# Optimization experiments

Measured on AMD Instinct MI355X. Metric: run time of the kernel, lower is better.

## Reference

```python
import jax, jax.numpy as jnp
import numpy as np

_EPS = 1e-6
B, N, W, R, NW = 64, 1024, 64, 4, 1


def _cosine_weights(memory, keys, strengths):
    # memory: [B,N,W], keys: [B,H,W], strengths: [B,H] -> [B,H,N]
    dot = jnp.einsum('bhw,bnw->bhn', keys, memory)
    mem_norm = jnp.sqrt(jnp.sum(memory * memory, axis=-1) + _EPS)  # [B,N]
    key_norm = jnp.sqrt(jnp.sum(keys * keys, axis=-1) + _EPS)      # [B,H]
    sim = dot / (key_norm[:, :, None] * mem_norm[:, None, :] + _EPS)
    sharp = sim * jax.nn.softplus(strengths)[:, :, None]
    return jax.nn.softmax(sharp, axis=-1)


def _allocation(usage):
    # usage: [B,N] -> allocation weights [B,N] (DNC sort-based free-list)
    usage = _EPS + (1.0 - _EPS) * usage
    nonusage = 1.0 - usage
    sorted_nonusage, indices = jax.lax.top_k(nonusage, N)
    sorted_usage = 1.0 - sorted_nonusage
    prod_excl = jnp.concatenate(
        [jnp.ones_like(sorted_usage[:, :1]), jnp.cumprod(sorted_usage[:, :-1], axis=-1)], axis=-1)
    sorted_alloc = sorted_nonusage * prod_excl
    inv_perm = jnp.argsort(indices, axis=-1)  # batch_invert_permutation
    return jnp.take_along_axis(sorted_alloc, inv_perm, axis=-1)  # batch_gather


def _forward(memory, prev_read_weights, prev_write_weights, prev_usage, prev_link,
             prev_precedence, read_keys, read_strengths, write_keys, write_strengths,
             write_vectors, erase_vectors, free_gate, alloc_gate, write_gate, read_mode):
    # ---- usage update (Freeness.call); prev write weights are stop-gradient'd ----
    ww = jax.lax.stop_gradient(prev_write_weights)
    agg_write = 1.0 - jnp.prod(1.0 - ww, axis=1)                       # [B,N]
    usage = prev_usage + (1.0 - prev_usage) * agg_write
    phi = jnp.prod(1.0 - free_gate[:, :, None] * prev_read_weights, axis=1)
    usage = usage * phi
    # ---- write weights: content + allocation ----
    write_content = _cosine_weights(memory, write_keys, write_strengths)  # [B,NW,N]
    wg = alloc_gate * write_gate                                          # [B,NW]
    allocs = []
    u = usage
    for i in range(NW):  # fixed small head loop
        a = _allocation(u)
        allocs.append(a)
        u = u + (1.0 - u) * wg[:, i:i + 1] * a
    alloc_w = jnp.stack(allocs, axis=1)                                   # [B,NW,N]
    ag = alloc_gate[:, :, None]
    write_weights = write_gate[:, :, None] * (ag * alloc_w + (1.0 - ag) * write_content)
    # ---- erase + write memory ----
    reset = jnp.prod(1.0 - write_weights[:, :, :, None] * erase_vectors[:, :, None, :], axis=1)
    memory_new = memory * reset + jnp.einsum('bwn,bwk->bnk', write_weights, write_vectors)
    # ---- temporal link matrix update ----
    wi = write_weights[:, :, :, None]   # [B,NW,N,1]
    wj = write_weights[:, :, None, :]   # [B,NW,1,N]
    new_link = (1.0 - wi - wj) * prev_link + wi * prev_precedence[:, :, None, :]
    link = new_link * (1.0 - jnp.eye(N, dtype=memory.dtype))[None, None]  # zero diagonal
    # (precedence update, part of new state; not needed for read_words output)
    precedence = (1.0 - jnp.sum(write_weights, axis=-1, keepdims=True)) * prev_precedence + write_weights
    del precedence
    # ---- read weights: content + directional (forward/backward along link) ----
    read_content = _cosine_weights(memory_new, read_keys, read_strengths)   # [B,R,N]
    fwd_w = jnp.einsum('brm,bwnm->brwn', prev_read_weights, link)           # adjoint_b=True
    bwd_w = jnp.einsum('brm,bwmn->brwn', prev_read_weights, link)
    mode = jax.nn.softmax(read_mode, axis=-1)                                # [B,R,2*NW+1]
    backward_mode = mode[:, :, :NW]
    forward_mode = mode[:, :, NW:2 * NW]
    content_mode = mode[:, :, 2 * NW]
    read_weights = (content_mode[:, :, None] * read_content
                    + jnp.einsum('brw,brwn->brn', forward_mode, fwd_w)
                    + jnp.einsum('brw,brwn->brn', backward_mode, bwd_w))
    read_words = jnp.einsum('brn,bnw->brw', read_weights, memory_new)        # [B,R,W]
    return read_words


def setup_inputs() -> dict:
    key = jax.random.key(0)
    ks = jax.random.split(key, 16)
    rn = lambda k, s: jax.random.normal(k, s, jnp.float32)
    ru = lambda k, s: jax.random.uniform(k, s, dtype=jnp.float32)
    return {
        'memory': rn(ks[0], (B, N, W)),
        'prev_read_weights': ru(ks[1], (B, R, N)),
        'prev_write_weights': ru(ks[2], (B, NW, N)),
        'prev_usage': ru(ks[3], (B, N)),
        'prev_link': ru(ks[4], (B, NW, N, N)),
        'prev_precedence': ru(ks[5], (B, NW, N)),
        'read_keys': rn(ks[6], (B, R, W)),
        'read_strengths': rn(ks[7], (B, R)),
        'write_keys': rn(ks[8], (B, NW, W)),
        'write_strengths': rn(ks[9], (B, NW)),
        'write_vectors': rn(ks[10], (B, NW, W)),
        'erase_vectors': ru(ks[11], (B, NW, W)),
        'free_gate': ru(ks[12], (B, R)),
        'alloc_gate': ru(ks[13], (B, NW)),
        'write_gate': ru(ks[14], (B, NW)),
        'read_mode': rn(ks[15], (B, R, 2 * NW + 1)),
    }


def reference(memory, prev_read_weights, prev_write_weights, prev_usage, prev_link,
              prev_precedence, read_keys, read_strengths, write_keys, write_strengths,
              write_vectors, erase_vectors, free_gate, alloc_gate, write_gate, read_mode):
    return _forward(memory, prev_read_weights, prev_write_weights, prev_usage, prev_link,
                    prev_precedence, read_keys, read_strengths, write_keys, write_strengths,
                    write_vectors, erase_vectors, free_gate, alloc_gate, write_gate, read_mode)
```

## Files before the change

kernel.cpp:

```cpp
#include <hip/hip_runtime.h>
#include <cmath>

#define NN 1024
#define BB 64
#define WD 64
#define RR 4

constexpr float EPSF = 1e-6f;

__device__ __forceinline__ float softplusf(float x) {
    return fmaxf(x, 0.f) + log1pf(expf(-fabsf(x)));
}

__device__ __forceinline__ float block_sum(float v, float* red, float* bc) {
#pragma unroll
    for (int o = 1; o < 64; o <<= 1) v += __shfl_xor(v, o, 64);
    const int wid = threadIdx.x >> 6, lane = threadIdx.x & 63;
    if (lane == 0) red[wid] = v;
    __syncthreads();
    if (wid == 0) {
        float x = (lane < 16) ? red[lane] : 0.f;
#pragma unroll
        for (int o = 1; o < 16; o <<= 1) x += __shfl_xor(x, o, 64);
        if (lane == 0) bc[0] = x;
    }
    __syncthreads();
    return bc[0];
}

__device__ __forceinline__ float block_max(float v, float* red, float* bc) {
#pragma unroll
    for (int o = 1; o < 64; o <<= 1) v = fmaxf(v, __shfl_xor(v, o, 64));
    const int wid = threadIdx.x >> 6, lane = threadIdx.x & 63;
    if (lane == 0) red[wid] = v;
    __syncthreads();
    if (wid == 0) {
        float x = (lane < 16) ? red[lane] : -INFINITY;
#pragma unroll
        for (int o = 1; o < 16; o <<= 1) x = fmaxf(x, __shfl_xor(x, o, 64));
        if (lane == 0) bc[0] = x;
    }
    __syncthreads();
    return bc[0];
}

__device__ __forceinline__ float4 block_sum4(float4 v, float4* red, float4* bc) {
#pragma unroll
    for (int o = 1; o < 64; o <<= 1) {
        v.x += __shfl_xor(v.x, o, 64); v.y += __shfl_xor(v.y, o, 64);
        v.z += __shfl_xor(v.z, o, 64); v.w += __shfl_xor(v.w, o, 64);
    }
    const int wid = threadIdx.x >> 6, lane = threadIdx.x & 63;
    if (lane == 0) red[wid] = v;
    __syncthreads();
    if (wid == 0) {
        float4 x;
        if (lane < 16) x = red[lane];
        else { x.x = 0.f; x.y = 0.f; x.z = 0.f; x.w = 0.f; }
#pragma unroll
        for (int o = 1; o < 16; o <<= 1) {
            x.x += __shfl_xor(x.x, o, 64); x.y += __shfl_xor(x.y, o, 64);
            x.z += __shfl_xor(x.z, o, 64); x.w += __shfl_xor(x.w, o, 64);
        }
        if (lane == 0) bc[0] = x;
    }
    __syncthreads();
    return bc[0];
}

__device__ __forceinline__ float4 block_max4(float4 v, float4* red, float4* bc) {
#pragma unroll
    for (int o = 1; o < 64; o <<= 1) {
        v.x = fmaxf(v.x, __shfl_xor(v.x, o, 64)); v.y = fmaxf(v.y, __shfl_xor(v.y, o, 64));
        v.z = fmaxf(v.z, __shfl_xor(v.z, o, 64)); v.w = fmaxf(v.w, __shfl_xor(v.w, o, 64));
    }
    const int wid = threadIdx.x >> 6, lane = threadIdx.x & 63;
    if (lane == 0) red[wid] = v;
    __syncthreads();
    if (wid == 0) {
        float4 x;
        if (lane < 16) x = red[lane];
        else { x.x = -INFINITY; x.y = -INFINITY; x.z = -INFINITY; x.w = -INFINITY; }
#pragma unroll
        for (int o = 1; o < 16; o <<= 1) {
            x.x = fmaxf(x.x, __shfl_xor(x.x, o, 64)); x.y = fmaxf(x.y, __shfl_xor(x.y, o, 64));
            x.z = fmaxf(x.z, __shfl_xor(x.z, o, 64)); x.w = fmaxf(x.w, __shfl_xor(x.w, o, 64));
        }
        if (lane == 0) bc[0] = x;
    }
    __syncthreads();
    return bc[0];
}

__global__ __launch_bounds__(1024) void prep_kernel(
    const float* __restrict__ memory, const float* __restrict__ prw,
    const float* __restrict__ pww, const float* __restrict__ pusage,
    const float* __restrict__ pprec,
    const float* __restrict__ rkeys_g, const float* __restrict__ rstr_g,
    const float* __restrict__ wkeys_g, const float* __restrict__ wstr_g,
    const float* __restrict__ wvec_g, const float* __restrict__ evec_g,
    const float* __restrict__ fg_g, const float* __restrict__ ag_g,
    const float* __restrict__ wg_g,
    float* __restrict__ wwG, float* __restrict__ rcG,
    float* __restrict__ SrpG, float* __restrict__ SuwwG)
{
    __shared__ float wkey[WD], wvecS[WD], evecS[WD], rkey[RR * WD];
    __shared__ float skey[NN];
    __shared__ int   sidx[NN];
    __shared__ float pArr[NN], wcArr[NN], allocArr[NN];
    __shared__ float red1[16], bc1[1];
    __shared__ float4 red4[16], bc4[1];

    const int b = blockIdx.x, tid = threadIdx.x, n = tid;

    if (tid < WD) {
        wkey[tid]  = wkeys_g[b * WD + tid];
        wvecS[tid] = wvec_g[b * WD + tid];
        evecS[tid] = evec_g[b * WD + tid];
    } else if (tid >= 128 && tid < 128 + RR * WD) {
        int k = tid - 128;
        rkey[k] = rkeys_g[b * RR * WD + k];
    }
    __syncthreads();

    float ur[RR];
#pragma unroll
    for (int r = 0; r < RR; ++r) ur[r] = prw[((size_t)b * RR + r) * NN + n];
    const float pw = pww[b * NN + n];
    const float pu = pusage[b * NN + n];
    float usage = pu + (1.f - pu) * pw;
    float phi = 1.f;
#pragma unroll
    for (int r = 0; r < RR; ++r) phi *= (1.f - fg_g[b * RR + r] * ur[r]);
    usage *= phi;

    const float* mrow = memory + ((size_t)b * NN + n) * WD;
    float dot = 0.f, nrm = 0.f, knrm = 0.f;
#pragma unroll 4
    for (int w4 = 0; w4 < WD / 4; ++w4) {
        const float4 m = *(const float4*)(mrow + w4 * 4);
        const float4 k = *(const float4*)(wkey + w4 * 4);
        dot  += m.x * k.x + m.y * k.y + m.z * k.z + m.w * k.w;
        nrm  += m.x * m.x + m.y * m.y + m.z * m.z + m.w * m.w;
        knrm += k.x * k.x + k.y * k.y + k.z * k.z + k.w * k.w;
    }
    const float sim = dot / (sqrtf(knrm + EPSF) * sqrtf(nrm + EPSF) + EPSF);
    const float sharp = sim * softplusf(wstr_g[b]);
    const float mxw = block_max(sharp, red1, bc1);
    const float exw = expf(sharp - mxw);
    const float smw = block_sum(exw, red1, bc1);
    wcArr[n] = exw / smw;

    const float ue = EPSF + (1.f - EPSF) * usage;
    skey[n] = 1.f - ue;
    sidx[n] = n;
    __syncthreads();
    for (int k = 2; k <= NN; k <<= 1) {
        for (int j = k >> 1; j > 0; j >>= 1) {
            const int ixj = tid ^ j;
            if (ixj > tid) {
                const float ka = skey[tid], kb = skey[ixj];
                const int ia = sidx[tid], ib = sidx[ixj];
                const bool precBA = (kb > ka) || (kb == ka && ib < ia);
                const bool precAB = (ka > kb) || (ka == kb && ia < ib);
                const bool dosw = ((tid & k) == 0) ? precBA : precAB;
                if (dosw) { skey[tid] = kb; skey[ixj] = ka; sidx[tid] = ib; sidx[ixj] = ia; }
            }
            __syncthreads();
        }
    }
    pArr[n] = (n == 0) ? 1.f : (1.f - skey[n - 1]);
    __syncthreads();
    for (int off = 1; off < NN; off <<= 1) {
        const float t = (n >= off) ? pArr[n - off] : 1.f;
        __syncthreads();
        pArr[n] *= t;
        __syncthreads();
    }
    allocArr[sidx[n]] = skey[n] * pArr[n];
    __syncthreads();

    const float agv = ag_g[b], wgv = wg_g[b];
    const float ww = wgv * (agv * allocArr[n] + (1.f - agv) * wcArr[n]);
    wwG[b * NN + n] = ww;

    float rdot0 = 0, rdot1 = 0, rdot2 = 0, rdot3 = 0, nn2 = 0;
    float rk0 = 0, rk1 = 0, rk2 = 0, rk3 = 0;
#pragma unroll 4
    for (int w4 = 0; w4 < WD / 4; ++w4) {
        const float4 m = *(const float4*)(mrow + w4 * 4);
        const float4 e = *(const float4*)(evecS + w4 * 4);
        const float4 v = *(const float4*)(wvecS + w4 * 4);
        float4 mn_;
        mn_.x = m.x * (1.f - ww * e.x) + ww * v.x;
        mn_.y = m.y * (1.f - ww * e.y) + ww * v.y;
        mn_.z = m.z * (1.f - ww * e.z) + ww * v.z;
        mn_.w = m.w * (1.f - ww * e.w) + ww * v.w;
        nn2 += mn_.x * mn_.x + mn_.y * mn_.y + mn_.z * mn_.z + mn_.w * mn_.w;
        const float4 k0 = *(const float4*)(rkey + 0 * WD + w4 * 4);
        const float4 k1 = *(const float4*)(rkey + 1 * WD + w4 * 4);
        const float4 k2 = *(const float4*)(rkey + 2 * WD + w4 * 4);
        const float4 k3 = *(const float4*)(rkey + 3 * WD + w4 * 4);
        rdot0 += k0.x * mn_.x + k0.y * mn_.y + k0.z * mn_.z + k0.w * mn_.w;
        rdot1 += k1.x * mn_.x + k1.y * mn_.y + k1.z * mn_.z + k1.w * mn_.w;
        rdot2 += k2.x * mn_.x + k2.y * mn_.y + k2.z * mn_.z + k2.w * mn_.w;
        rdot3 += k3.x * mn_.x + k3.y * mn_.y + k3.z * mn_.z + k3.w * mn_.w;
        rk0 += k0.x * k0.x + k0.y * k0.y + k0.z * k0.z + k0.w * k0.w;
        rk1 += k1.x * k1.x + k1.y * k1.y + k1.z * k1.z + k1.w * k1.w;
        rk2 += k2.x * k2.x + k2.y * k2.y + k2.z * k2.z + k2.w * k2.w;
        rk3 += k3.x * k3.x + k3.y * k3.y + k3.z * k3.z + k3.w * k3.w;
    }
    const float mnn = sqrtf(nn2 + EPSF);
    float4 sharp4;
    sharp4.x = rdot0 / (sqrtf(rk0 + EPSF) * mnn + EPSF) * softplusf(rstr_g[b * RR + 0]);
    sharp4.y = rdot1 / (sqrtf(rk1 + EPSF) * mnn + EPSF) * softplusf(rstr_g[b * RR + 1]);
    sharp4.z = rdot2 / (sqrtf(rk2 + EPSF) * mnn + EPSF) * softplusf(rstr_g[b * RR + 2]);
    sharp4.w = rdot3 / (sqrtf(rk3 + EPSF) * mnn + EPSF) * softplusf(rstr_g[b * RR + 3]);
    const float4 mx4 = block_max4(sharp4, red4, bc4);
    float4 e4;
    e4.x = expf(sharp4.x - mx4.x); e4.y = expf(sharp4.y - mx4.y);
    e4.z = expf(sharp4.z - mx4.z); e4.w = expf(sharp4.w - mx4.w);
    const float4 s4 = block_sum4(e4, red4, bc4);
    rcG[((size_t)b * RR + 0) * NN + n] = e4.x / s4.x;
    rcG[((size_t)b * RR + 1) * NN + n] = e4.y / s4.y;
    rcG[((size_t)b * RR + 2) * NN + n] = e4.z / s4.z;
    rcG[((size_t)b * RR + 3) * NN + n] = e4.w / s4.w;

    const float prec_n = pprec[b * NN + n];
    float4 sp4, sw4;
    sp4.x = ur[0] * prec_n; sp4.y = ur[1] * prec_n; sp4.z = ur[2] * prec_n; sp4.w = ur[3] * prec_n;
    const float4 SrpV = block_sum4(sp4, red4, bc4);
    sw4.x = ur[0] * ww; sw4.y = ur[1] * ww; sw4.z = ur[2] * ww; sw4.w = ur[3] * ww;
    const float4 SuwwV = block_sum4(sw4, red4, bc4);
    if (tid == 0) {
        SrpG[b * RR + 0] = SrpV.x; SrpG[b * RR + 1] = SrpV.y;
        SrpG[b * RR + 2] = SrpV.z; SrpG[b * RR + 3] = SrpV.w;
        SuwwG[b * RR + 0] = SuwwV.x; SuwwG[b * RR + 1] = SuwwV.y;
        SuwwG[b * RR + 2] = SuwwV.z; SuwwG[b * RR + 3] = SuwwV.w;
    }
}

__global__ __launch_bounds__(256) void link_kernel(
    const float* __restrict__ L, const float* __restrict__ prw,
    const float* __restrict__ wwG,
    float* __restrict__ rowU, float* __restrict__ rowV,
    float* __restrict__ colU, float* __restrict__ colV)
{
    __shared__ float uL[RR * NN];
    __shared__ float uwL[RR * NN];
    __shared__ float tile[64 * 68];

    const int b = blockIdx.y;
    const int n0 = blockIdx.x * 64;
    const int t = threadIdx.x;
    const int lane = t & 63;
    const int wid = t >> 6;

    for (int k = t; k < RR * NN; k += 256) {
        const float u = prw[(size_t)b * RR * NN + k];
        uL[k] = u;
        uwL[k] = u * wwG[b * NN + (k & (NN - 1))];
    }
    __syncthreads();

    const float* Lb = L + (size_t)b * NN * NN;
    float fuA = 0.f, fvA = 0.f;

    for (int tIdx = 0; tIdx < 16; ++tIdx) {
        const int m0 = tIdx * 64;
#pragma unroll
        for (int k = 0; k < 4; ++k) {
            const int f4 = t + k * 256;
            const int row = f4 >> 4, c4 = f4 & 15;
            const float4 v = *(const float4*)&Lb[(size_t)(n0 + row) * NN + m0 + c4 * 4];
            *(float4*)&tile[row * 68 + c4 * 4] = v;
        }
        __syncthreads();

#pragma unroll 4
        for (int g = 0; g < 16; ++g) {
            const float4 v  = *(const float4*)&tile[lane * 68 + g * 4];
            const float4 u  = *(const float4*)&uL[wid * NN + m0 + g * 4];
            const float4 uw = *(const float4*)&uwL[wid * NN + m0 + g * 4];
            fuA += v.x * u.x + v.y * u.y + v.z * u.z + v.w * u.w;
            fvA += v.x * uw.x + v.y * uw.y + v.z * uw.z + v.w * uw.w;
        }

        float cu = 0.f, cv = 0.f;
#pragma unroll 4
        for (int n4 = 0; n4 < 16; ++n4) {
            const float4 u  = *(const float4*)&uL[wid * NN + n0 + n4 * 4];
            const float4 uw = *(const float4*)&uwL[wid * NN + n0 + n4 * 4];
            const float v0 = tile[(n4 * 4 + 0) * 68 + lane];
            const float v1 = tile[(n4 * 4 + 1) * 68 + lane];
            const float v2 = tile[(n4 * 4 + 2) * 68 + lane];
            const float v3 = tile[(n4 * 4 + 3) * 68 + lane];
            cu += v0 * u.x + v1 * u.y + v2 * u.z + v3 * u.w;
            cv += v0 * uw.x + v1 * uw.y + v2 * uw.z + v3 * uw.w;
        }
        unsafeAtomicAdd(&colU[((size_t)b * RR + wid) * NN + m0 + lane], cu);
        unsafeAtomicAdd(&colV[((size_t)b * RR + wid) * NN + m0 + lane], cv);
        __syncthreads();
    }
    rowU[((size_t)b * RR + wid) * NN + n0 + lane] = fuA;
    rowV[((size_t)b * RR + wid) * NN + n0 + lane] = fvA;
}

__global__ __launch_bounds__(256) void combine_kernel(
    const float* __restrict__ memory, const float* __restrict__ prw,
    const float* __restrict__ pprec, const float* __restrict__ L,
    const float* __restrict__ evec_g, const float* __restrict__ wvec_g,
    const float* __restrict__ rmode_g,
    const float* __restrict__ wwG, const float* __restrict__ rcG,
    const float* __restrict__ rowU, const float* __restrict__ rowV,
    const float* __restrict__ colU, const float* __restrict__ colV,
    const float* __restrict__ SrpG, const float* __restrict__ SuwwG,
    float* __restrict__ out)
{
    __shared__ float rwL[RR][256];
    __shared__ float wwS[256];

    const int b = blockIdx.y;
    const int n0 = blockIdx.x * 256;
    const int t = threadIdx.x;
    const int n = n0 + t;

    const float wwn = wwG[b * NN + n];
    wwS[t] = wwn;
    const float prec_n = pprec[b * NN + n];
    const float diag = L[(size_t)b * NN * NN + (size_t)n * (NN + 1)];

#pragma unroll
    for (int r = 0; r < RR; ++r) {
        const size_t idx = ((size_t)b * RR + r) * NN + n;
        const float un = prw[idx];
        const float rc = rcG[idx];
        const float ru = rowU[idx], rv = rowV[idx];
        const float cuv = colU[idx], cvv = colV[idx];
        const float Srp = SrpG[b * RR + r], Suww = SuwwG[b * RR + r];
        const float corr = un * (1.f - 2.f * wwn) * diag;
        const float fwd = (1.f - wwn) * ru - rv - corr + wwn * (Srp - un * prec_n);
        const float bwd = (1.f - wwn) * cuv - cvv - corr + prec_n * (Suww - un * wwn);
        const float m0 = rmode_g[((size_t)b * RR + r) * 3 + 0];
        const float m1 = rmode_g[((size_t)b * RR + r) * 3 + 1];
        const float m2 = rmode_g[((size_t)b * RR + r) * 3 + 2];
        const float mx = fmaxf(m0, fmaxf(m1, m2));
        const float e0 = expf(m0 - mx), e1 = expf(m1 - mx), e2 = expf(m2 - mx);
        const float inv = 1.f / (e0 + e1 + e2);
        rwL[r][t] = (e2 * inv) * rc + (e1 * inv) * fwd + (e0 * inv) * bwd;
    }
    __syncthreads();

    const int r = t >> 6, w = t & 63;
    const float ev = evec_g[b * WD + w], wv = wvec_g[b * WD + w];
    float acc = 0.f;
    const float* mb = memory + ((size_t)b * NN + n0) * WD;
#pragma unroll 8
    for (int i = 0; i < 256; ++i) {
        const float m = mb[(size_t)i * WD + w];
        const float wwi = wwS[i];
        const float mn_ = m * (1.f - wwi * ev) + wwi * wv;
        acc += rwL[r][i] * mn_;
    }
    unsafeAtomicAdd(&out[((size_t)b * RR + r) * WD + w], acc);
}

extern "C" void kernel_launch(void* const* d_in, const int* in_sizes, int n_in,
                              void* d_out, int out_size, void* d_ws, size_t ws_size,
                              hipStream_t stream) {
    const float* memory = (const float*)d_in[0];
    const float* prw    = (const float*)d_in[1];
    const float* pww    = (const float*)d_in[2];
    const float* pusage = (const float*)d_in[3];
    const float* plink  = (const float*)d_in[4];
    const float* pprec  = (const float*)d_in[5];
    const float* rkeys  = (const float*)d_in[6];
    const float* rstr   = (const float*)d_in[7];
    const float* wkeys  = (const float*)d_in[8];
    const float* wstr   = (const float*)d_in[9];
    const float* wvec   = (const float*)d_in[10];
    const float* evec   = (const float*)d_in[11];
    const float* fg     = (const float*)d_in[12];
    const float* ag     = (const float*)d_in[13];
    const float* wg     = (const float*)d_in[14];
    const float* rmode  = (const float*)d_in[15];

    float* ws = (float*)d_ws;
    const size_t BN  = (size_t)BB * NN;
    const size_t BRN = (size_t)BB * RR * NN;
    float* wwG  = ws;
    float* rcG  = wwG + BN;
    float* rowU = rcG + BRN;
    float* rowV = rowU + BRN;
    float* colU = rowV + BRN;
    float* colV = colU + BRN;
    float* Srp  = colV + BRN;
    float* Suww = Srp + (size_t)BB * RR;

    hipMemsetAsync(colU, 0, 2 * BRN * sizeof(float), stream);
    hipMemsetAsync(d_out, 0, (size_t)out_size * sizeof(float), stream);

    prep_kernel<<<BB, 1024, 0, stream>>>(memory, prw, pww, pusage, pprec,
                                         rkeys, rstr, wkeys, wstr, wvec, evec,
                                         fg, ag, wg, wwG, rcG, Srp, Suww);
    link_kernel<<<dim3(16, BB), 256, 0, stream>>>(plink, prw, wwG,
                                                  rowU, rowV, colU, colV);
    combine_kernel<<<dim3(4, BB), 256, 0, stream>>>(memory, prw, pprec, plink,
                                                    evec, wvec, rmode,
                                                    wwG, rcG, rowU, rowV, colU, colV,
                                                    Srp, Suww, (float*)d_out);
}
```

Baseline: 596.1 us.

## Restructure link kernel into register-accumulated stripes with per-stripe column partials

```diff
diff --git a/kernel.cpp b/kernel.cpp
--- a/kernel.cpp
+++ b/kernel.cpp
@@ -5,11 +5,16 @@
 #define BB 64
 #define WD 64
 #define RR 4
+#define STRIPES 16
 
 constexpr float EPSF = 1e-6f;
 
 __device__ __forceinline__ float softplusf(float x) {
     return fmaxf(x, 0.f) + log1pf(expf(-fabsf(x)));
+}
+
+__device__ __forceinline__ float rfl(float x) {
+    return __int_as_float(__builtin_amdgcn_readfirstlane(__float_as_int(x)));
 }
 
 __device__ __forceinline__ float block_sum(float v, float* red, float* bc) {
@@ -101,7 +106,8 @@
     const float* __restrict__ wvec_g, const float* __restrict__ evec_g,
     const float* __restrict__ fg_g, const float* __restrict__ ag_g,
     const float* __restrict__ wg_g,
-    float* __restrict__ wwG, float* __restrict__ rcG,
+    float* __restrict__ wwG, float* __restrict__ uwGout,
+    float* __restrict__ rcG,
     float* __restrict__ SrpG, float* __restrict__ SuwwG)
 {
     __shared__ float wkey[WD], wvecS[WD], evecS[WD], rkey[RR * WD];
@@ -183,6 +189,9 @@
     const float agv = ag_g[b], wgv = wg_g[b];
     const float ww = wgv * (agv * allocArr[n] + (1.f - agv) * wcArr[n]);
     wwG[b * NN + n] = ww;
+#pragma unroll
+    for (int r = 0; r < RR; ++r)
+        uwGout[((size_t)b * RR + r) * NN + n] = ur[r] * ww;
 
     float rdot0 = 0, rdot1 = 0, rdot2 = 0, rdot3 = 0, nn2 = 0;
     float rk0 = 0, rk1 = 0, rk2 = 0, rk3 = 0;
@@ -240,70 +249,103 @@
     }
 }
 
-__global__ __launch_bounds__(256) void link_kernel(
+__global__ __launch_bounds__(1024) void link_kernel(
     const float* __restrict__ L, const float* __restrict__ prw,
-    const float* __restrict__ wwG,
-    float* __restrict__ rowU, float* __restrict__ rowV,
-    float* __restrict__ colU, float* __restrict__ colV)
+    const float* __restrict__ uwG,
+    float* __restrict__ rowP, float* __restrict__ colPart)
 {
-    __shared__ float uL[RR * NN];
-    __shared__ float uwL[RR * NN];
-    __shared__ float tile[64 * 68];
-
-    const int b = blockIdx.y;
-    const int n0 = blockIdx.x * 64;
-    const int t = threadIdx.x;
-    const int lane = t & 63;
-    const int wid = t >> 6;
-
-    for (int k = t; k < RR * NN; k += 256) {
-        const float u = prw[(size_t)b * RR * NN + k];
-        uL[k] = u;
-        uwL[k] = u * wwG[b * NN + (k & (NN - 1))];
-    }
-    __syncthreads();
-
-    const float* Lb = L + (size_t)b * NN * NN;
-    float fuA = 0.f, fvA = 0.f;
-
-    for (int tIdx = 0; tIdx < 16; ++tIdx) {
-        const int m0 = tIdx * 64;
-#pragma unroll
-        for (int k = 0; k < 4; ++k) {
-            const int f4 = t + k * 256;
-            const int row = f4 >> 4, c4 = f4 & 15;
-            const float4 v = *(const float4*)&Lb[(size_t)(n0 + row) * NN + m0 + c4 * 4];
-            *(float4*)&tile[row * 68 + c4 * 4] = v;
-        }
+    __shared__ float smem[16384];
+
+    const int s = blockIdx.x, b = blockIdx.y;
+    const int t = threadIdx.x, lane = t & 63, wid = t >> 6;
+
+#pragma unroll
+    for (int k = 0; k < 8; ++k) smem[t + k * 1024] = 0.f;
+    __syncthreads();
+
+    const int n0 = s * 64;
+    const int nb = n0 + wid * 4;
+
+    const float* vp[8];
+#pragma unroll
+    for (int r = 0; r < RR; ++r) {
+        vp[r]      = prw + (((size_t)b * RR + r) << 10);
+        vp[4 + r]  = uwG + (((size_t)b * RR + r) << 10);
+    }
+
+    float us[4][8];
+#pragma unroll
+    for (int rr = 0; rr < 4; ++rr)
+#pragma unroll
+        for (int v = 0; v < 8; ++v)
+            us[rr][v] = rfl(vp[v][nb + rr]);
+
+    float racc[4][8];
+#pragma unroll
+    for (int rr = 0; rr < 4; ++rr)
+#pragma unroll
+        for (int v = 0; v < 8; ++v) racc[rr][v] = 0.f;
+
+    const float* Lb = L + ((size_t)b << 20);
+
+    for (int cc = 0; cc < 16; ++cc) {
+        const int c = (cc + wid) & 15;
+        const int col = (c << 6) + lane;
+
+        float ul[8];
+#pragma unroll
+        for (int v = 0; v < 8; ++v) ul[v] = vp[v][col];
+
+        float cacc[8] = {0.f, 0.f, 0.f, 0.f, 0.f, 0.f, 0.f, 0.f};
+#pragma unroll
+        for (int rr = 0; rr < 4; ++rr) {
+            const float val = Lb[((size_t)(nb + rr) << 10) + col];
+#pragma unroll
+            for (int v = 0; v < 8; ++v) racc[rr][v] = fmaf(val, ul[v], racc[rr][v]);
+#pragma unroll
+            for (int v = 0; v < 8; ++v) cacc[v] = fmaf(val, us[rr][v], cacc[v]);
+        }
+#pragma unroll
+        for (int v = 0; v < 8; ++v)
+            unsafeAtomicAdd(&smem[(v << 10) + col], cacc[v]);
+    }
+    __syncthreads();
+
+    {
+        const size_t base = (((size_t)s * BB + b) * 8) << 10;
+#pragma unroll
+        for (int v = 0; v < 8; ++v)
+            colPart[base + (v << 10) + t] = smem[(v << 10) + t];
+    }
+    __syncthreads();
+
+#pragma unroll
+    for (int rd = 0; rd < 2; ++rd) {
+#pragma unroll
+        for (int row2 = 0; row2 < 2; ++row2)
+#pragma unroll
+            for (int v = 0; v < 8; ++v) {
+                const int q = row2 * 8 + v;
+                smem[(wid << 10) + (q << 6) + (lane ^ q)] = racc[rd * 2 + row2][v];
+            }
         __syncthreads();
-
-#pragma unroll 4
-        for (int g = 0; g < 16; ++g) {
-            const float4 v  = *(const float4*)&tile[lane * 68 + g * 4];
-            const float4 u  = *(const float4*)&uL[wid * NN + m0 + g * 4];
-            const float4 uw = *(const float4*)&uwL[wid * NN + m0 + g * 4];
-            fuA += v.x * u.x + v.y * u.y + v.z * u.z + v.w * u.w;
-            fvA += v.x * uw.x + v.y * uw.y + v.z * uw.z + v.w * uw.w;
-        }
-
-        float cu = 0.f, cv = 0.f;
-#pragma unroll 4
-        for (int n4 = 0; n4 < 16; ++n4) {
-            const float4 u  = *(const float4*)&uL[wid * NN + n0 + n4 * 4];
-            const float4 uw = *(const float4*)&uwL[wid * NN + n0 + n4 * 4];
-            const float v0 = tile[(n4 * 4 + 0) * 68 + lane];
-            const float v1 = tile[(n4 * 4 + 1) * 68 + lane];
-            const float v2 = tile[(n4 * 4 + 2) * 68 + lane];
-            const float v3 = tile[(n4 * 4 + 3) * 68 + lane];
-            cu += v0 * u.x + v1 * u.y + v2 * u.z + v3 * u.w;
-            cv += v0 * uw.x + v1 * uw.y + v2 * uw.z + v3 * uw.w;
-        }
-        unsafeAtomicAdd(&colU[((size_t)b * RR + wid) * NN + m0 + lane], cu);
-        unsafeAtomicAdd(&colV[((size_t)b * RR + wid) * NN + m0 + lane], cv);
+        const int q = lane >> 2;
+        const int sub = lane & 3;
+        float sum = 0.f;
+#pragma unroll
+        for (int i = 0; i < 16; ++i) {
+            const int j = sub * 16 + i;
+            sum += smem[(wid << 10) + (q << 6) + (j ^ q)];
+        }
+        sum += __shfl_xor(sum, 1, 64);
+        sum += __shfl_xor(sum, 2, 64);
+        if (sub == 0) {
+            const int v = q & 7, row2 = q >> 3;
+            const int n = n0 + wid * 4 + rd * 2 + row2;
+            rowP[(((size_t)b * 8 + v) << 10) + n] = sum;
+        }
         __syncthreads();
     }
-    rowU[((size_t)b * RR + wid) * NN + n0 + lane] = fuA;
-    rowV[((size_t)b * RR + wid) * NN + n0 + lane] = fvA;
 }
 
 __global__ __launch_bounds__(256) void combine_kernel(
@@ -312,8 +354,7 @@
     const float* __restrict__ evec_g, const float* __restrict__ wvec_g,
     const float* __restrict__ rmode_g,
     const float* __restrict__ wwG, const float* __restrict__ rcG,
-    const float* __restrict__ rowU, const float* __restrict__ rowV,
-    const float* __restrict__ colU, const float* __restrict__ colV,
+    const float* __restrict__ rowP, const float* __restrict__ colPart,
     const float* __restrict__ SrpG, const float* __restrict__ SuwwG,
     float* __restrict__ out)
 {
@@ -335,8 +376,15 @@
         const size_t idx = ((size_t)b * RR + r) * NN + n;
         const float un = prw[idx];
         const float rc = rcG[idx];
-        const float ru = rowU[idx], rv = rowV[idx];
-        const float cuv = colU[idx], cvv = colV[idx];
+        const float ru = rowP[(((size_t)b * 8 + r) << 10) + n];
+        const float rv = rowP[(((size_t)b * 8 + 4 + r) << 10) + n];
+        float cuv = 0.f, cvv = 0.f;
+#pragma unroll
+        for (int s2 = 0; s2 < STRIPES; ++s2) {
+            const size_t base = (((size_t)s2 * BB + b) * 8) << 10;
+            cuv += colPart[base + ((size_t)r << 10) + n];
+            cvv += colPart[base + ((size_t)(4 + r) << 10) + n];
+        }
         const float Srp = SrpG[b * RR + r], Suww = SuwwG[b * RR + r];
         const float corr = un * (1.f - 2.f * wwn) * diag;
         const float fwd = (1.f - wwn) * ru - rv - corr + wwn * (Srp - un * prec_n);
@@ -360,7 +408,7 @@
         const float m = mb[(size_t)i * WD + w];
         const float wwi = wwS[i];
         const float mn_ = m * (1.f - wwi * ev) + wwi * wv;
-        acc += rwL[r][i] * mn_;
+        acc = fmaf(rwL[r][i], mn_, acc);
     }
     unsafeAtomicAdd(&out[((size_t)b * RR + r) * WD + w], acc);
 }
@@ -386,27 +434,28 @@
     const float* rmode  = (const float*)d_in[15];
 
     float* ws = (float*)d_ws;
-    const size_t BN  = (size_t)BB * NN;
-    const size_t BRN = (size_t)BB * RR * NN;
+    const size_t BN   = (size_t)BB * NN;
+    const size_t BRN  = (size_t)BB * RR * NN;
+    const size_t ROWP = (size_t)BB * 8 * NN;
+    const size_t COLP = (size_t)STRIPES * BB * 8 * NN;
+
     float* wwG  = ws;
-    float* rcG  = wwG + BN;
-    float* rowU = rcG + BRN;
-    float* rowV = rowU + BRN;
-    float* colU = rowV + BRN;
-    float* colV = colU + BRN;
-    float* Srp  = colV + BRN;
+    float* uwG  = wwG + BN;
+    float* rcG  = uwG + BRN;
+    float* rowP = rcG + BRN;
+    float* colP = rowP + ROWP;
+    float* Srp  = colP + COLP;
     float* Suww = Srp + (size_t)BB * RR;
 
-    hipMemsetAsync(colU, 0, 2 * BRN * sizeof(float), stream);
     hipMemsetAsync(d_out, 0, (size_t)out_size * sizeof(float), stream);
 
     prep_kernel<<<BB, 1024, 0, stream>>>(memory, prw, pww, pusage, pprec,
                                          rkeys, rstr, wkeys, wstr, wvec, evec,
-                                         fg, ag, wg, wwG, rcG, Srp, Suww);
-    link_kernel<<<dim3(16, BB), 256, 0, stream>>>(plink, prw, wwG,
-                                                  rowU, rowV, colU, colV);
+                                         fg, ag, wg, wwG, uwG, rcG, Srp, Suww);
+    link_kernel<<<dim3(STRIPES, BB), 1024, 0, stream>>>(plink, prw, uwG,
+                                                        rowP, colP);
     combine_kernel<<<dim3(4, BB), 256, 0, stream>>>(memory, prw, pprec, plink,
                                                     evec, wvec, rmode,
-                                                    wwG, rcG, rowU, rowV, colU, colV,
+                                                    wwG, rcG, rowP, colP,
                                                     Srp, Suww, (float*)d_out);
 }
```

New measurement: 1.133 ms. +90.1%, slower.
